# Kernel tuning notes

Hardware: AMD Instinct MI355X
Metric: run time of the kernel (lower is better)

The kernel has to match this reference:

```python
import jax, jax.numpy as jnp
import numpy as np

N_NODES = 200000
N_EDGES = 6400000
F_OUT = 128
N_GRAPHS = 64


def setup_inputs() -> dict:
    key = jax.random.key(0)
    ks = jax.random.split(key, 6)
    x = jax.random.normal(ks[0], (N_NODES, 1), dtype=jnp.float32)
    edge_index = jax.random.randint(ks[1], (2, N_EDGES), 0, N_NODES, dtype=jnp.int64)
    batch = jnp.sort(jax.random.randint(ks[2], (N_NODES,), 0, N_GRAPHS, dtype=jnp.int64))
    edge_weights = jax.random.uniform(ks[3], (N_EDGES,), dtype=jnp.float32)
    W_l = jax.random.normal(ks[4], (F_OUT, 1), dtype=jnp.float32)
    b_l = jnp.zeros((F_OUT,), dtype=jnp.float32)
    W_r = jax.random.normal(ks[5], (F_OUT, 1), dtype=jnp.float32)
    return {"x": x, "edge_index": edge_index, "batch": batch,
            "edge_weights": edge_weights, "W_l": W_l, "b_l": b_l, "W_r": W_r}


def reference(x, edge_index, batch, edge_weights, W_l, b_l, W_r):
    # SAGEConv (mean aggregation, edge-weighted messages as in PyG propagate):
    #   out_i = lin_l( mean_{j in N(i)} w_ij * x_j ) + lin_r(x_i)
    n = x.shape[0]
    src, dst = edge_index[0], edge_index[1]
    msgs = x[src] * edge_weights[:, None]                      # [E, 1] gather
    agg_sum = jax.ops.segment_sum(msgs, dst, num_segments=n)  # [N, 1] scatter-add
    deg = jax.ops.segment_sum(jnp.ones((src.shape[0],), x.dtype), dst, num_segments=n)
    agg = agg_sum / jnp.maximum(deg, 1.0)[:, None]             # mean
    h = agg @ W_l.T + b_l + x @ W_r.T                          # [N, F_OUT]
    # dropout(p=0.2) is identity in eval mode -> omitted
    out = jax.ops.segment_max(h, batch, num_segments=N_GRAPHS)  # global_max_pool
    return out
```

## Files before the change

kernel.cpp:

```cpp
#include <hip/hip_runtime.h>
#include <hip/hip_bf16.h>
#include <float.h>
#include <math.h>

constexpr int NN = 200000;
constexpr int NE = 6400000;
constexpr int FO = 128;
constexpr int NG = 64;

constexpr int NCHUNK = 512;
constexpr int CHUNK  = NE / NCHUNK;
constexpr int C4     = CHUNK / 4;
constexpr int BNODES = 1024;
constexpr int NBUK   = (NN + BNODES - 1) / BNODES;

constexpr float Q_SCALE = 4096.0f;
constexpr float Q_INV   = 1.0f / 4096.0f;

__device__ __forceinline__ unsigned encf(float f) {
    unsigned u = __float_as_uint(f);
    return (u & 0x80000000u) ? ~u : (u | 0x80000000u);
}
__device__ __forceinline__ float decf(unsigned e) {
    unsigned u = (e & 0x80000000u) ? (e & 0x7FFFFFFFu) : ~e;
    return __uint_as_float(u);
}

__global__ void k_hist(const int* __restrict__ ei, unsigned* __restrict__ cnt,
                       unsigned* __restrict__ out_enc,
                       const int* __restrict__ batch, int* __restrict__ start) {
    __shared__ unsigned h[NBUK];
    int c = blockIdx.x, tid = threadIdx.x;
    for (int i = tid; i < NBUK; i += 1024) h[i] = 0u;
    if (c == 0) for (int i = tid; i < NG * FO; i += 1024) out_enc[i] = encf(-INFINITY);
    if (c == 1 && tid <= NG) {
        if (tid == NG) start[tid] = NN;
        else {
            int lo = 0, hi = NN;
            while (lo < hi) { int mid = (lo + hi) >> 1; if (batch[mid] < tid) lo = mid + 1; else hi = mid; }
            start[tid] = lo;
        }
    }
    __syncthreads();
    const int4* d4 = (const int4*)(ei + NE + c * CHUNK);
#pragma unroll
    for (int k = 0; k < 4; ++k) {
        int idx = tid + k * 1024;
        if (idx < C4) {
            int4 v = d4[idx];
            atomicAdd(&h[v.x >> 10], 1u);
            atomicAdd(&h[v.y >> 10], 1u);
            atomicAdd(&h[v.z >> 10], 1u);
            atomicAdd(&h[v.w >> 10], 1u);
        }
    }
    __syncthreads();
    for (int i = tid; i < NBUK; i += 1024) cnt[i * NCHUNK + c] = h[i];
}

__global__ void k_scanA(unsigned* __restrict__ cnt, unsigned* __restrict__ T) {
    __shared__ unsigned s[NCHUNK];
    int b = blockIdx.x, t = threadIdx.x;
    unsigned v = cnt[b * NCHUNK + t];
    s[t] = v;
    __syncthreads();
    for (int off = 1; off < NCHUNK; off <<= 1) {
        unsigned u = (t >= off) ? s[t - off] : 0u;
        __syncthreads();
        s[t] += u;
        __syncthreads();
    }
    cnt[b * NCHUNK + t] = s[t] - v;
    if (t == NCHUNK - 1) T[b] = s[t];
}

__global__ void k_scanB(const unsigned* __restrict__ T, unsigned* __restrict__ B) {
    __shared__ unsigned s[256];
    int t = threadIdx.x;
    unsigned v = (t < NBUK) ? T[t] : 0u;
    s[t] = v;
    __syncthreads();
    for (int off = 1; off < 256; off <<= 1) {
        unsigned u = (t >= off) ? s[t - off] : 0u;
        __syncthreads();
        s[t] += u;
        __syncthreads();
    }
    if (t < NBUK) B[t] = s[t] - v;
    if (t == 255) B[NBUK] = s[255];
}

__global__ void k_place(const int* __restrict__ ei, const float* __restrict__ x,
                        const float* __restrict__ w,
                        const unsigned* __restrict__ cnt,
                        const unsigned* __restrict__ B,
                        unsigned* __restrict__ rec,
                        int blo, int bhi, unsigned cap) {
    __shared__ unsigned offs[NBUK];
    int c = blockIdx.x, tid = threadIdx.x;
    unsigned b0 = B[blo];
    for (int b = blo + tid; b < bhi; b += 1024)
        offs[b] = B[b] - b0 + cnt[b * NCHUNK + c];
    __syncthreads();
    const int4*   s4 = (const int4*)(ei + c * CHUNK);
    const int4*   d4 = (const int4*)(ei + NE + c * CHUNK);
    const float4* w4 = (const float4*)(w + c * CHUNK);
#pragma unroll
    for (int k = 0; k < 4; ++k) {
        int idx = tid + k * 1024;
        if (idx >= C4) continue;
        int4   sv = s4[idx];
        int4   dv = d4[idx];
        float4 wv = w4[idx];
        int    ds[4] = {dv.x, dv.y, dv.z, dv.w};
        int    ss[4] = {sv.x, sv.y, sv.z, sv.w};
        float  wf[4] = {wv.x, wv.y, wv.z, wv.w};
#pragma unroll
        for (int j = 0; j < 4; ++j) {
            int d = ds[j], b = d >> 10;
            if (b < blo || b >= bhi) continue;
            float m = x[ss[j]] * wf[j];
            int q = __float2int_rn(m * Q_SCALE) + 32768;
            q = min(max(q, 0), 65535);
            unsigned slot = atomicAdd(&offs[b], 1u);
            if (slot < cap)
                rec[slot] = ((unsigned)(d & (BNODES - 1)) << 16) | (unsigned)q;
        }
    }
}

__global__ void k_bucket(const unsigned* __restrict__ rec,
                         const unsigned* __restrict__ B,
                         float* __restrict__ mean, int blo) {
    __shared__ unsigned long long acc[BNODES];
    int b = blo + blockIdx.x, tid = threadIdx.x;
    for (int i = tid; i < BNODES; i += 1024) acc[i] = 0ull;
    __syncthreads();
    unsigned b0 = B[blo];
    unsigned r0 = B[b] - b0, r1 = B[b + 1] - b0;
    for (unsigned r = r0 + tid; r < r1; r += 1024) {
        unsigned v = rec[r];
        atomicAdd(&acc[v >> 16], (1ull << 48) | (unsigned long long)(v & 0xFFFFu));
    }
    __syncthreads();
    int n0 = b * BNODES;
    for (int i = tid; i < BNODES; i += 1024) {
        int n = n0 + i;
        if (n < NN) {
            unsigned long long a = acc[i];
            float cn = (float)(unsigned)(a >> 48);
            float sq = (float)(a & 0xFFFFFFFFFFFFull);
            float sum = (sq - 32768.0f * cn) * Q_INV;
            mean[n] = sum / fmaxf(cn, 1.0f);
        }
    }
}

constexpr int SPLITS = 16;
__global__ void k_max8(const float* __restrict__ mean, const float* __restrict__ x,
                       const float* __restrict__ Wl, const float* __restrict__ Wr,
                       const int* __restrict__ start, unsigned* __restrict__ out_enc) {
    int g = blockIdx.x;
    int lo = start[g], hi = start[g + 1];
    int len = hi - lo;
    if (len <= 0) return;
    int per = (len + gridDim.y - 1) / gridDim.y;
    int a0 = lo + blockIdx.y * per;
    int a1 = min(a0 + per, hi);
    if (a0 >= a1) return;
    int f = threadIdx.x;
    float wl = Wl[f], wr = Wr[f];
    float m0 = -INFINITY, m1 = -INFINITY;
    int i = a0;
    for (; i + 2 <= a1; i += 2) {
        m0 = fmaxf(m0, fmaf(mean[i],     wl, x[i]     * wr));
        m1 = fmaxf(m1, fmaf(mean[i + 1], wl, x[i + 1] * wr));
    }
    if (i < a1) m0 = fmaxf(m0, fmaf(mean[i], wl, x[i] * wr));
    atomicMax(&out_enc[g * FO + f], encf(fmaxf(m0, m1)));
}

__global__ void k_decode(const unsigned* __restrict__ out_enc,
                         const float* __restrict__ bl, float* __restrict__ out) {
    int i = blockIdx.x * blockDim.x + threadIdx.x;
    if (i >= NG * FO) return;
    out[i] = decf(out_enc[i]) + bl[i & (FO - 1)];
}

constexpr float FP_SCALE = 16777216.0f;
constexpr float FP_INV   = 1.0f / FP_SCALE;
__device__ __forceinline__ unsigned long long pack_msg(float m) {
    return (1ull << 48) + (unsigned long long)(__float2ll_rn(m * FP_SCALE) + (1ll << 30));
}
__global__ void k_init1(unsigned long long* __restrict__ agg, unsigned* __restrict__ out_enc,
                        const int* __restrict__ batch, int* __restrict__ start) {
    int i = blockIdx.x * blockDim.x + threadIdx.x;
    if (i < NN) agg[i] = 0ull;
    if (i < NG * FO) out_enc[i] = encf(-INFINITY);
    if (i <= NG) {
        if (i == NG) start[i] = NN;
        else {
            int lo = 0, hi = NN;
            while (lo < hi) { int mid = (lo + hi) >> 1; if (batch[mid] < i) lo = mid + 1; else hi = mid; }
            start[i] = lo;
        }
    }
}
__global__ void k_scatter1(const int* __restrict__ ei, const float* __restrict__ x,
                           const float* __restrict__ w, unsigned long long* __restrict__ agg) {
    int t = blockIdx.x * blockDim.x + threadIdx.x;
    int e0 = t * 4;
    if (e0 >= NE) return;
    int4 sv = *(const int4*)(ei + e0);
    int4 dv = *(const int4*)(ei + NE + e0);
    float4 wv = *(const float4*)(w + e0);
    atomicAdd(&agg[dv.x], pack_msg(x[sv.x] * wv.x));
    atomicAdd(&agg[dv.y], pack_msg(x[sv.y] * wv.y));
    atomicAdd(&agg[dv.z], pack_msg(x[sv.z] * wv.z));
    atomicAdd(&agg[dv.w], pack_msg(x[sv.w] * wv.w));
}
__global__ void k_max1(const unsigned long long* __restrict__ agg, const float* __restrict__ x,
                       const float* __restrict__ Wl, const float* __restrict__ Wr,
                       const int* __restrict__ start, unsigned* __restrict__ out_enc) {
    int g = blockIdx.x;
    int lo = start[g], hi = start[g + 1];
    if (hi - lo <= 0) return;
    int per = (hi - lo + gridDim.y - 1) / gridDim.y;
    int a0 = lo + blockIdx.y * per, a1 = min(a0 + per, hi);
    if (a0 >= a1) return;
    int f = threadIdx.x;
    float wl = Wl[f], wr = Wr[f], m = -INFINITY;
    for (int i = a0; i < a1; ++i) {
        unsigned long long v = agg[i];
        int cnt = (int)(v >> 48);
        long long sfp = (long long)(v & 0xFFFFFFFFFFFFull) - ((long long)cnt << 30);
        float av = ((float)sfp * FP_INV) / fmaxf((float)cnt, 1.0f);
        m = fmaxf(m, fmaf(av, wl, x[i] * wr));
    }
    atomicMax(&out_enc[g * FO + f], encf(m));
}

extern "C" void kernel_launch(void* const* d_in, const int* in_sizes, int n_in,
                              void* d_out, int out_size, void* d_ws, size_t ws_size,
                              hipStream_t stream) {
    const float* x  = (const float*)d_in[0];
    const int*   ei = (const int*)d_in[1];
    const int*   bt = (const int*)d_in[2];
    const float* ew = (const float*)d_in[3];
    const float* Wl = (const float*)d_in[4];
    const float* bl = (const float*)d_in[5];
    const float* Wr = (const float*)d_in[6];
    float* out = (float*)d_out;
    char* ws = (char*)d_ws;

    const size_t FIXED = (size_t)NBUK * NCHUNK * 4
                       + 1024
                       + 1024
                       + 800000
                       + 32768
                       + 512
                       + 256;
    int nphase = 0;
    unsigned cap = 0;
    for (int p = 1; p <= 3; ++p) {
        unsigned c = (unsigned)(NE / p) + 16384u;
        if (ws_size >= FIXED + (size_t)c * 4) { nphase = p; cap = c; break; }
    }

    if (nphase) {
        size_t off = 0;
        unsigned* rec  = (unsigned*)(ws + off); off += (size_t)cap * 4;          off = (off + 15) & ~15ull;
        unsigned* cnt  = (unsigned*)(ws + off); off += (size_t)NBUK * NCHUNK * 4; off = (off + 15) & ~15ull;
        unsigned* T    = (unsigned*)(ws + off); off += 1024;
        unsigned* B    = (unsigned*)(ws + off); off += 1024;
        float*    mean = (float*)(ws + off);    off += 800000;                   off = (off + 15) & ~15ull;
        unsigned* out_enc = (unsigned*)(ws + off); off += 32768;
        int*      start   = (int*)(ws + off);

        k_hist<<<NCHUNK, 1024, 0, stream>>>(ei, cnt, out_enc, bt, start);
        k_scanA<<<NBUK, NCHUNK, 0, stream>>>(cnt, T);
        k_scanB<<<1, 256, 0, stream>>>(T, B);
        int per = (NBUK + nphase - 1) / nphase;
        for (int p = 0; p < nphase; ++p) {
            int blo = p * per;
            int bhi = min(blo + per, NBUK);
            if (blo >= bhi) break;
            k_place<<<NCHUNK, 1024, 0, stream>>>(ei, x, ew, cnt, B, rec, blo, bhi, cap);
            k_bucket<<<bhi - blo, 1024, 0, stream>>>(rec, B, mean, blo);
        }
        k_max8<<<dim3(NG, SPLITS), FO, 0, stream>>>(mean, x, Wl, Wr, start, out_enc);
        k_decode<<<(NG * FO + 255) / 256, 256, 0, stream>>>(out_enc, bl, out);
    } else {
        unsigned long long* agg = (unsigned long long*)ws;
        unsigned* out_enc = (unsigned*)(ws + 1600000);
        int*      start   = (int*)(ws + 1600000 + 32768);
        k_init1<<<(NN + 255) / 256, 256, 0, stream>>>(agg, out_enc, bt, start);
        k_scatter1<<<(NE / 4 + 255) / 256, 256, 0, stream>>>(ei, x, ew, agg);
        k_max1<<<dim3(NG, 32), FO, 0, stream>>>(agg, x, Wl, Wr, start, out_enc);
        k_decode<<<(NG * FO + 255) / 256, 256, 0, stream>>>(out_enc, bl, out);
    }
}
```

Measured before the change: 97.87 us.

## Stage bucket records in shared memory before coalesced global write

k_place now computes per-chunk bucket sizes and a local prefix scan, scatters records into a shared-memory buffer grouped by bucket, and then copies them to global memory in contiguous runs, using a binary search to find each record's bucket. The aim is to replace scattered 4-byte global stores with coalesced writes. It adds a 50KB shared buffer per block, which lowers occupancy, plus extra syncs and a scan. Launch bounds of 1024 are also added to three kernels.

Result: faster. 89.47 us (-8.6%).

```diff
diff --git a/kernel.cpp b/kernel.cpp
--- a/kernel.cpp
+++ b/kernel.cpp
@@ -26,7 +26,7 @@
     return __uint_as_float(u);
 }
 
-__global__ void k_hist(const int* __restrict__ ei, unsigned* __restrict__ cnt,
+__global__ __launch_bounds__(1024) void k_hist(const int* __restrict__ ei, unsigned* __restrict__ cnt,
                        unsigned* __restrict__ out_enc,
                        const int* __restrict__ batch, int* __restrict__ start) {
     __shared__ unsigned h[NBUK];
@@ -90,18 +90,41 @@
     if (t == 255) B[NBUK] = s[255];
 }
 
-__global__ void k_place(const int* __restrict__ ei, const float* __restrict__ x,
+__global__ __launch_bounds__(1024) void k_place(const int* __restrict__ ei, const float* __restrict__ x,
                         const float* __restrict__ w,
                         const unsigned* __restrict__ cnt,
+                        const unsigned* __restrict__ T,
                         const unsigned* __restrict__ B,
                         unsigned* __restrict__ rec,
                         int blo, int bhi, unsigned cap) {
-    __shared__ unsigned offs[NBUK];
+    __shared__ unsigned lincl[256];
+    __shared__ unsigned loffs[NBUK];
+    __shared__ unsigned gbase[NBUK];
+    __shared__ unsigned recbuf[CHUNK];
     int c = blockIdx.x, tid = threadIdx.x;
-    unsigned b0 = B[blo];
-    for (int b = blo + tid; b < bhi; b += 1024)
-        offs[b] = B[b] - b0 + cnt[b * NCHUNK + c];
-    __syncthreads();
+    int nb = bhi - blo;
+
+    unsigned sz = 0;
+    if (tid < nb) {
+        int b = blo + tid;
+        unsigned pre = cnt[b * NCHUNK + c];
+        unsigned nxt = (c + 1 < NCHUNK) ? cnt[b * NCHUNK + c + 1] : T[b];
+        sz = nxt - pre;
+        gbase[b] = B[b] - B[blo] + pre;
+    }
+    if (tid < 256) lincl[tid] = sz;
+    __syncthreads();
+    for (int off = 1; off < 256; off <<= 1) {
+        unsigned v = 0;
+        if (tid < 256 && tid >= off) v = lincl[tid - off];
+        __syncthreads();
+        if (tid < 256) lincl[tid] += v;
+        __syncthreads();
+    }
+    if (tid < nb) loffs[blo + tid] = lincl[tid] - sz;
+    __syncthreads();
+    unsigned nrec = lincl[nb - 1];
+
     const int4*   s4 = (const int4*)(ei + c * CHUNK);
     const int4*   d4 = (const int4*)(ei + NE + c * CHUNK);
     const float4* w4 = (const float4*)(w + c * CHUNK);
@@ -122,14 +145,22 @@
             float m = x[ss[j]] * wf[j];
             int q = __float2int_rn(m * Q_SCALE) + 32768;
             q = min(max(q, 0), 65535);
-            unsigned slot = atomicAdd(&offs[b], 1u);
-            if (slot < cap)
-                rec[slot] = ((unsigned)(d & (BNODES - 1)) << 16) | (unsigned)q;
-        }
-    }
-}
-
-__global__ void k_bucket(const unsigned* __restrict__ rec,
+            unsigned lslot = atomicAdd(&loffs[b], 1u);
+            recbuf[lslot] = ((unsigned)(d & (BNODES - 1)) << 16) | (unsigned)q;
+        }
+    }
+    __syncthreads();
+
+    for (unsigned i = tid; i < nrec; i += 1024) {
+        int lo = 0, hi = nb;
+        while (lo < hi) { int mid = (lo + hi) >> 1; if (lincl[mid] <= i) lo = mid + 1; else hi = mid; }
+        unsigned excl = lo ? lincl[lo - 1] : 0u;
+        unsigned g = gbase[blo + lo] + (i - excl);
+        if (g < cap) rec[g] = recbuf[i];
+    }
+}
+
+__global__ __launch_bounds__(1024) void k_bucket(const unsigned* __restrict__ rec,
                          const unsigned* __restrict__ B,
                          float* __restrict__ mean, int blo) {
     __shared__ unsigned long long acc[BNODES];
@@ -285,7 +316,7 @@
             int blo = p * per;
             int bhi = min(blo + per, NBUK);
             if (blo >= bhi) break;
-            k_place<<<NCHUNK, 1024, 0, stream>>>(ei, x, ew, cnt, B, rec, blo, bhi, cap);
+            k_place<<<NCHUNK, 1024, 0, stream>>>(ei, x, ew, cnt, T, B, rec, blo, bhi, cap);
             k_bucket<<<bhi - blo, 1024, 0, stream>>>(rec, B, mean, blo);
         }
         k_max8<<<dim3(NG, SPLITS), FO, 0, stream>>>(mean, x, Wl, Wr, start, out_enc);
```
